# Kernel optimization log

Hardware: AMD Instinct MI355X
Metric: run time of the kernel (lower is better)

## Reference

```python
import jax, jax.numpy as jnp
import numpy as np

B, M, D = 8, 1024, 1024
H = 16
HD = D // H  # 64
F = 4096

def layer_norm(x, gamma, beta, eps=1e-5):
    mu = jnp.mean(x, axis=-1, keepdims=True)
    var = jnp.var(x, axis=-1, keepdims=True)
    return (x - mu) * jax.lax.rsqrt(var + eps) * gamma + beta

def setup_inputs() -> dict:
    key = jax.random.key(0)
    ks = jax.random.split(key, 16)
    s = 0.02
    return {
        "h": jax.random.normal(ks[0], (B, M, D), jnp.float32),
        "h_all": jax.random.normal(ks[1], (B, M, D), jnp.float32),
        "Wq": jax.random.normal(ks[2], (D, D), jnp.float32) * s,
        "Wk": jax.random.normal(ks[3], (D, D), jnp.float32) * s,
        "Wv": jax.random.normal(ks[4], (D, D), jnp.float32) * s,
        "Wo": jax.random.normal(ks[5], (D, D), jnp.float32) * s,
        "W1": jax.random.normal(ks[6], (D, F), jnp.float32) * s,
        "b1": jnp.zeros((F,), jnp.float32),
        "W2": jax.random.normal(ks[7], (F, D), jnp.float32) * s,
        "b2": jnp.zeros((D,), jnp.float32),
        "g1": jnp.ones((D,), jnp.float32),
        "be1": jnp.zeros((D,), jnp.float32),
        "g2": jnp.ones((D,), jnp.float32),
        "be2": jnp.zeros((D,), jnp.float32),
    }

def reference(h, h_all, Wq, Wk, Wv, Wo, W1, b1, W2, b2, g1, be1, g2, be2):
    Bx, Mx, Dx = h.shape
    # projections (no bias, per nn.Linear(bias=False))
    q = (h @ Wq).reshape(Bx, Mx, H, HD)        # [B,M,H,hd]
    k = (h_all @ Wk).reshape(Bx, -1, H, HD)    # [B,N,H,hd]
    v = (h_all @ Wv).reshape(Bx, -1, H, HD)
    # attention: scale by sqrt(head_dim) as in SeqAttention(hidden_size=head_dim)
    scores = jnp.einsum('bqhd,bkhd->bhqk', q, k) / jnp.sqrt(jnp.float32(HD))
    attn = jax.nn.softmax(scores, axis=-1)
    ctx = jnp.einsum('bhqk,bkhd->bqhd', attn, v).reshape(Bx, Mx, Dx)
    attn_out = ctx @ Wo
    # post-norm residual 1
    h1 = layer_norm(h + attn_out, g1, be1)
    # FFN
    ff = jax.nn.relu(h1 @ W1 + b1) @ W2 + b2
    # post-norm residual 2
    out = layer_norm(h1 + ff, g2, be2)
    return out
```

## Files before the change

### kernel.cpp

```cpp
#include <hip/hip_runtime.h>
#include <hip/hip_bf16.h>

#define ROWS 8192
#define DD   1024
#define HH   16
#define HD   64
#define FF   4096

typedef __attribute__((ext_vector_type(4))) float f32x4;
typedef __attribute__((ext_vector_type(8))) __bf16 bf16x8;
typedef __attribute__((ext_vector_type(8))) short short8v;

static __device__ __forceinline__ unsigned short f2bf(float f) {
  unsigned u = __float_as_uint(f);
  u += 0x7fffu + ((u >> 16) & 1u);
  return (unsigned short)(u >> 16);
}

static __device__ __forceinline__ f32x4 mfma16(bf16x8 a, bf16x8 b, f32x4 c) {
  return __builtin_amdgcn_mfma_f32_16x16x32_bf16(a, b, c, 0, 0, 0);
}

#define GLOAD16(gp, lp) __builtin_amdgcn_global_load_lds( \
    (__attribute__((address_space(1))) void*)(gp), \
    (__attribute__((address_space(3))) void*)(lp), 16, 0, 0)

__global__ __launch_bounds__(256) void cast_bf16_k(
    const float* __restrict__ in, unsigned short* __restrict__ out, int n4) {
  int i = blockIdx.x * 256 + threadIdx.x;
  if (i >= n4) return;
  float4 v = ((const float4*)in)[i];
  ushort4 o;
  o.x = f2bf(v.x); o.y = f2bf(v.y); o.z = f2bf(v.z); o.w = f2bf(v.w);
  ((ushort4*)out)[i] = o;
}

__global__ __launch_bounds__(256) void transpose_cast_k(
    const float* __restrict__ in, unsigned short* __restrict__ out, int R, int C) {
  __shared__ float tile[32][33];
  int bx = blockIdx.x * 32;
  int by = blockIdx.y * 32;
  int tx = threadIdx.x, ty = threadIdx.y;
  #pragma unroll
  for (int i = 0; i < 32; i += 8)
    tile[ty + i][tx] = in[(size_t)(by + ty + i) * C + bx + tx];
  __syncthreads();
  #pragma unroll
  for (int i = 0; i < 32; i += 8)
    out[(size_t)(bx + ty + i) * R + by + tx] = f2bf(tile[tx][ty + i]);
}

template <int BM, int MODE>
__global__ __launch_bounds__(512, 2) void gemm256(
    const unsigned short* __restrict__ A, const unsigned short* __restrict__ BT,
    const float* __restrict__ bias, void* __restrict__ Cout,
    int Ni, int Ki, int nbx) {
  constexpr int LA = BM / 64;
  constexpr int MR = BM / 32;
  constexpr int VN = LA + 4;
  __shared__ unsigned short As[2][BM * 64];
  __shared__ unsigned short Bs[2][256 * 64];

  const int tid  = threadIdx.x;
  const int lane = tid & 63;
  const int wid  = tid >> 6;
  const int wm   = wid >> 2;
  const int wn   = wid & 3;
  const int lr   = lane & 15;
  const int kq   = lane >> 4;
  const int axor = (lr & 7) << 4;

  const int nwg = gridDim.x;
  const int cpx = nwg >> 3;
  const int wg  = (int)blockIdx.x;
  const int swz = (wg & 7) * cpx + (wg >> 3);
  const int bx = swz % nbx, by = swz / nbx;
  const int brow = by * BM, bcol = bx * 256;

  const int srow = wid * 8 + (lane >> 3);
  const int scol = ((lane & 7) * 8) ^ ((srow & 7) << 3);
  size_t offA[LA], offB[4];
  #pragma unroll
  for (int L = 0; L < LA; ++L)
    offA[L] = (size_t)(brow + L * 64 + srow) * Ki + scol;
  #pragma unroll
  for (int L = 0; L < 4; ++L)
    offB[L] = (size_t)(bcol + L * 64 + srow) * Ki + scol;

  auto stage = [&](int t, int d) {
    #pragma unroll
    for (int L = 0; L < LA; ++L)
      GLOAD16(A + offA[L] + t * 64, (char*)As[d] + L * 8192 + wid * 1024);
    #pragma unroll
    for (int L = 0; L < 4; ++L)
      GLOAD16(BT + offB[L] + t * 64, (char*)Bs[d] + L * 8192 + wid * 1024);
  };

  f32x4 acc[MR][4] = {};
  const int NT = Ki >> 6;

  stage(0, 0);
  stage(1, 1);

  #pragma unroll 1
  for (int t = 0; t < NT; ++t) {
    const int d = t & 1;
    if constexpr (BM == 256) asm volatile("s_waitcnt vmcnt(8)" ::: "memory");
    else                     asm volatile("s_waitcnt vmcnt(6)" ::: "memory");
    __builtin_amdgcn_s_barrier();
    __builtin_amdgcn_sched_barrier(0);

    const unsigned short* as = As[d];
    const unsigned short* bs = Bs[d];
    #pragma unroll
    for (int kk = 0; kk < 2; ++kk) {
      bf16x8 af[MR], bfv[4];
      #pragma unroll
      for (int m = 0; m < MR; ++m)
        af[m] = *(const bf16x8*)((const char*)as +
            (wm * (BM / 2) + m * 16 + lr) * 128 + ((kk * 64 + kq * 16) ^ axor));
      #pragma unroll
      for (int n = 0; n < 4; ++n)
        bfv[n] = *(const bf16x8*)((const char*)bs +
            (wn * 64 + n * 16 + lr) * 128 + ((kk * 64 + kq * 16) ^ axor));
      #pragma unroll
      for (int m = 0; m < MR; ++m)
        #pragma unroll
        for (int n = 0; n < 4; ++n)
          acc[m][n] = mfma16(af[m], bfv[n], acc[m][n]);
    }

    __builtin_amdgcn_s_barrier();
    __builtin_amdgcn_sched_barrier(0);
    const int ts = (t + 2 < NT) ? t + 2 : NT - 1;
    stage(ts, d);
  }

  #pragma unroll
  for (int m = 0; m < MR; ++m) {
    #pragma unroll
    for (int n = 0; n < 4; ++n) {
      const int r0 = brow + wm * (BM / 2) + m * 16 + kq * 4;
      const int c  = bcol + wn * 64 + n * 16 + lr;
      const float bv = (MODE == 2 || MODE == 3) ? bias[c] : 0.0f;
      #pragma unroll
      for (int e = 0; e < 4; ++e) {
        float v = acc[m][n][e] + bv;
        if (MODE == 2) v = fmaxf(v, 0.0f);
        if (MODE == 0 || MODE == 2)
          ((unsigned short*)Cout)[(size_t)(r0 + e) * Ni + c] = f2bf(v);
        else
          ((float*)Cout)[(size_t)(r0 + e) * Ni + c] = v;
      }
    }
  }
}

__global__ __launch_bounds__(256, 2) void attn_k(
    const unsigned short* __restrict__ q, const unsigned short* __restrict__ kv,
    unsigned short* __restrict__ ctx) {
  __shared__ unsigned short Ks[64 * 64];
  __shared__ unsigned short Vt[64 * 64];
  __shared__ unsigned short Ps[4][16 * 64];
  const int tid = threadIdx.x;
  const int lane = tid & 63;
  const int wid = tid >> 6;
  const int bh = blockIdx.y;
  const int b = bh >> 4, h = bh & 15;
  const int qrow0 = blockIdx.x * 64 + wid * 16;
  const size_t tokbase = (size_t)b * 1024;

  bf16x8 aq[2];
  {
    const unsigned short* qp =
        q + (size_t)(tokbase + qrow0 + (lane & 15)) * DD + h * 64 + (lane >> 4) * 8;
    aq[0] = *(const bf16x8*)qp;
    aq[1] = *(const bf16x8*)(qp + 32);
  }

  float l_part[4] = {0.f, 0.f, 0.f, 0.f};
  f32x4 acc[4] = {};
  const float C = 0.125f * 1.4426950408889634f;

  for (int kt = 0; kt < 16; ++kt) {
    __syncthreads();
    #pragma unroll
    for (int it = 0; it < 2; ++it) {
      int r = (it * 4 + wid) * 8 + (lane >> 3);
      int cb = ((lane & 7) * 8) ^ ((r & 7) << 3);
      GLOAD16(kv + (size_t)(tokbase + kt * 64 + r) * 2048 + h * 64 + cb,
              (char*)Ks + (it * 4 + wid) * 1024);
    }
    #pragma unroll
    for (int it = 0; it < 2; ++it) {
      int tok = it * 32 + (tid >> 3);
      int d0 = (tid & 7) * 8;
      short8v vv = *(const short8v*)(kv + (size_t)(tokbase + kt * 64 + tok) * 2048 +
                                     1024 + h * 64 + d0);
      #pragma unroll
      for (int e = 0; e < 8; ++e) {
        int d = d0 + e;
        int sw = ((d & 7) ^ ((d >> 3) & 7)) & 7;
        *(unsigned short*)((char*)Vt + (((d * 128 + tok * 2) ^ (sw << 4)))) =
            (unsigned short)vv[e];
      }
    }
    __syncthreads();

    f32x4 sv[4] = {};
    #pragma unroll
    for (int jb = 0; jb < 4; ++jb)
      #pragma unroll
      for (int ks = 0; ks < 2; ++ks) {
        int row = jb * 16 + (lane & 15);
        bf16x8 bk = *(const bf16x8*)((const char*)Ks +
            ((row * 128 + ks * 64 + (lane >> 4) * 16) ^ ((row & 7) << 4)));
        sv[jb] = mfma16(aq[ks], bk, sv[jb]);
      }

    #pragma unroll
    for (int jb = 0; jb < 4; ++jb)
      #pragma unroll
      for (int j = 0; j < 4; ++j) {
        float p = exp2f(sv[jb][j] * C);
        sv[jb][j] = p;
        l_part[j] += p;
      }

    #pragma unroll
    for (int jb = 0; jb < 4; ++jb)
      #pragma unroll
      for (int j = 0; j < 4; ++j) {
        int row = (lane >> 4) * 4 + j;
        *(unsigned short*)((char*)Ps[wid] +
            ((row * 128 + (jb * 16 + (lane & 15)) * 2) ^ ((row & 7) << 4))) =
            f2bf(sv[jb][j]);
      }

    #pragma unroll
    for (int ks = 0; ks < 2; ++ks) {
      int prow = lane & 15;
      bf16x8 ap = *(const bf16x8*)((const char*)Ps[wid] +
          ((prow * 128 + ks * 64 + (lane >> 4) * 16) ^ ((prow & 7) << 4)));
      #pragma unroll
      for (int db = 0; db < 4; ++db) {
        int d = db * 16 + (lane & 15);
        int sw = ((d & 7) ^ ((d >> 3) & 7)) & 7;
        bf16x8 bv = *(const bf16x8*)((const char*)Vt +
            ((d * 128 + ks * 64 + (lane >> 4) * 16) ^ (sw << 4)));
        acc[db] = mfma16(ap, bv, acc[db]);
      }
    }
  }

  #pragma unroll
  for (int j = 0; j < 4; ++j) {
    float l = l_part[j];
    #pragma unroll
    for (int mk = 1; mk < 16; mk <<= 1) l += __shfl_xor(l, mk);
    float inv = 1.0f / l;
    int r = qrow0 + (lane >> 4) * 4 + j;
    #pragma unroll
    for (int db = 0; db < 4; ++db)
      ctx[(size_t)(tokbase + r) * DD + h * 64 + db * 16 + (lane & 15)] =
          f2bf(acc[db][j] * inv);
  }
}

template <int WB>
__global__ __launch_bounds__(256) void ln_add_k(
    const float* __restrict__ a, const float* __restrict__ b,
    const float* __restrict__ gamma, const float* __restrict__ beta,
    float* __restrict__ outf, unsigned short* __restrict__ outb) {
  int row = blockIdx.x;
  int tid = threadIdx.x;
  size_t base = (size_t)row * 1024 + tid * 4;
  float4 va = *(const float4*)(a + base);
  float4 vb = *(const float4*)(b + base);
  float x[4] = {va.x + vb.x, va.y + vb.y, va.z + vb.z, va.w + vb.w};
  float s = x[0] + x[1] + x[2] + x[3];
  float sq = x[0] * x[0] + x[1] * x[1] + x[2] * x[2] + x[3] * x[3];
  #pragma unroll
  for (int mk = 1; mk < 64; mk <<= 1) {
    s += __shfl_xor(s, mk);
    sq += __shfl_xor(sq, mk);
  }
  __shared__ float red[8];
  int wid = tid >> 6, lane = tid & 63;
  if (lane == 0) { red[wid] = s; red[4 + wid] = sq; }
  __syncthreads();
  s = red[0] + red[1] + red[2] + red[3];
  sq = red[4] + red[5] + red[6] + red[7];
  float mu = s * (1.0f / 1024.0f);
  float var = sq * (1.0f / 1024.0f) - mu * mu;
  float rs = rsqrtf(var + 1e-5f);
  float4 g = *(const float4*)(gamma + tid * 4);
  float4 be = *(const float4*)(beta + tid * 4);
  float y[4];
  y[0] = (x[0] - mu) * rs * g.x + be.x;
  y[1] = (x[1] - mu) * rs * g.y + be.y;
  y[2] = (x[2] - mu) * rs * g.z + be.z;
  y[3] = (x[3] - mu) * rs * g.w + be.w;
  float4 o; o.x = y[0]; o.y = y[1]; o.z = y[2]; o.w = y[3];
  *(float4*)(outf + base) = o;
  if (WB) {
    ushort4 ob;
    ob.x = f2bf(y[0]); ob.y = f2bf(y[1]); ob.z = f2bf(y[2]); ob.w = f2bf(y[3]);
    *(ushort4*)(outb + base) = ob;
  }
}

extern "C" void kernel_launch(void* const* d_in, const int* in_sizes, int n_in,
                              void* d_out, int out_size, void* d_ws, size_t ws_size,
                              hipStream_t stream) {
  const float* h    = (const float*)d_in[0];
  const float* hall = (const float*)d_in[1];
  const float* Wq   = (const float*)d_in[2];
  const float* Wk   = (const float*)d_in[3];
  const float* Wv   = (const float*)d_in[4];
  const float* Wo   = (const float*)d_in[5];
  const float* W1   = (const float*)d_in[6];
  const float* b1   = (const float*)d_in[7];
  const float* W2   = (const float*)d_in[8];
  const float* b2   = (const float*)d_in[9];
  const float* g1   = (const float*)d_in[10];
  const float* be1  = (const float*)d_in[11];
  const float* g2   = (const float*)d_in[12];
  const float* be2  = (const float*)d_in[13];

  char* ws = (char*)d_ws;
  size_t off = 0;
  auto alloc = [&](size_t n) { size_t o = off; off += (n + 255) & ~(size_t)255; return o; };
  const size_t hb_o   = alloc((size_t)ROWS * DD * 2);
  const size_t hab_o  = alloc((size_t)ROWS * DD * 2);
  const size_t wqt_o  = alloc((size_t)DD * DD * 2);
  const size_t wkvt_o = alloc((size_t)DD * DD * 4);
  const size_t wot_o  = alloc((size_t)DD * DD * 2);
  const size_t w1t_o  = alloc((size_t)DD * FF * 2);
  const size_t w2t_o  = alloc((size_t)FF * DD * 2);
  const size_t qb_o   = alloc((size_t)ROWS * DD * 2);
  const size_t kvb_o  = alloc((size_t)ROWS * DD * 4);
  const size_t cx_o   = alloc((size_t)ROWS * DD * 2);
  const size_t h1_o   = alloc((size_t)ROWS * DD * 4);
  const size_t h1b_o  = alloc((size_t)ROWS * DD * 2);

  unsigned short* hb   = (unsigned short*)(ws + hb_o);
  unsigned short* hab  = (unsigned short*)(ws + hab_o);
  unsigned short* wqt  = (unsigned short*)(ws + wqt_o);
  unsigned short* wkvt = (unsigned short*)(ws + wkvt_o);
  unsigned short* wot  = (unsigned short*)(ws + wot_o);
  unsigned short* w1t  = (unsigned short*)(ws + w1t_o);
  unsigned short* w2t  = (unsigned short*)(ws + w2t_o);
  unsigned short* qb   = (unsigned short*)(ws + qb_o);
  unsigned short* kvb  = (unsigned short*)(ws + kvb_o);
  unsigned short* cxb  = (unsigned short*)(ws + cx_o);
  float*          h1   = (float*)(ws + h1_o);
  unsigned short* h1b  = (unsigned short*)(ws + h1b_o);
  float*          attn_out = (float*)(ws + hb_o);
  unsigned short* ff1      = (unsigned short*)(ws + qb_o);
  float*          outf     = (float*)d_out;

  cast_bf16_k<<<ROWS * DD / 1024, 256, 0, stream>>>(h, hb, ROWS * DD / 4);
  cast_bf16_k<<<ROWS * DD / 1024, 256, 0, stream>>>(hall, hab, ROWS * DD / 4);
  dim3 tb(32, 8);
  transpose_cast_k<<<dim3(32, 32), tb, 0, stream>>>(Wq, wqt, DD, DD);
  transpose_cast_k<<<dim3(32, 32), tb, 0, stream>>>(Wk, wkvt, DD, DD);
  transpose_cast_k<<<dim3(32, 32), tb, 0, stream>>>(Wv, wkvt + (size_t)DD * DD, DD, DD);
  transpose_cast_k<<<dim3(32, 32), tb, 0, stream>>>(Wo, wot, DD, DD);
  transpose_cast_k<<<dim3(128, 32), tb, 0, stream>>>(W1, w1t, DD, FF);
  transpose_cast_k<<<dim3(32, 128), tb, 0, stream>>>(W2, w2t, FF, DD);

  gemm256<128, 0><<<dim3(64 * 4), 512, 0, stream>>>(hb,  wqt,  nullptr, qb,  DD,   DD, 4);
  gemm256<256, 0><<<dim3(32 * 8), 512, 0, stream>>>(hab, wkvt, nullptr, kvb, 2048, DD, 8);

  attn_k<<<dim3(16, 128), 256, 0, stream>>>(qb, kvb, cxb);

  gemm256<128, 1><<<dim3(64 * 4), 512, 0, stream>>>(cxb, wot, nullptr, attn_out, DD, DD, 4);
  ln_add_k<1><<<ROWS, 256, 0, stream>>>(h, attn_out, g1, be1, h1, h1b);

  gemm256<256, 2><<<dim3(32 * 16), 512, 0, stream>>>(h1b, w1t, b1, ff1, FF, DD, 16);
  gemm256<128, 3><<<dim3(64 * 4),  512, 0, stream>>>(ff1, w2t, b2, outf, DD, FF, 4);

  ln_add_k<0><<<ROWS, 256, 0, stream>>>(h1, outf, g2, be2, outf, nullptr);
}
```

Measured before the change: 411.9 us.

## Write V transposed from the KV GEMM and double-buffer K/V loads in attention

The KV projection GEMM gets a new epilogue mode that writes K row-major and V transposed per (batch, head) into separate buffers. This lets the attention kernel stage both K and V with async global-to-LDS loads instead of scalar LDS transposes. The attention kernel now uses 512-thread blocks covering 128 query rows, double-buffers K/V tiles with prefetch two steps ahead, and synchronises with explicit waitcnt and barriers. An lgkmcnt wait is also added before the GEMM barrier. The transposed V stores are 8-byte scattered writes, and the larger LDS footprint may limit occupancy.

```diff
diff --git a/kernel.cpp b/kernel.cpp
--- a/kernel.cpp
+++ b/kernel.cpp
@@ -9,7 +9,6 @@
 
 typedef __attribute__((ext_vector_type(4))) float f32x4;
 typedef __attribute__((ext_vector_type(8))) __bf16 bf16x8;
-typedef __attribute__((ext_vector_type(8))) short short8v;
 
 static __device__ __forceinline__ unsigned short f2bf(float f) {
   unsigned u = __float_as_uint(f);
@@ -53,11 +52,10 @@
 template <int BM, int MODE>
 __global__ __launch_bounds__(512, 2) void gemm256(
     const unsigned short* __restrict__ A, const unsigned short* __restrict__ BT,
-    const float* __restrict__ bias, void* __restrict__ Cout,
+    const float* __restrict__ bias, void* __restrict__ Cout, void* __restrict__ Cout2,
     int Ni, int Ki, int nbx) {
   constexpr int LA = BM / 64;
   constexpr int MR = BM / 32;
-  constexpr int VN = LA + 4;
   __shared__ unsigned short As[2][BM * 64];
   __shared__ unsigned short Bs[2][256 * 64];
 
@@ -130,6 +128,7 @@
           acc[m][n] = mfma16(af[m], bfv[n], acc[m][n]);
     }
 
+    asm volatile("s_waitcnt lgkmcnt(0)" ::: "memory");
     __builtin_amdgcn_s_barrier();
     __builtin_amdgcn_sched_barrier(0);
     const int ts = (t + 2 < NT) ? t + 2 : NT - 1;
@@ -142,38 +141,65 @@
     for (int n = 0; n < 4; ++n) {
       const int r0 = brow + wm * (BM / 2) + m * 16 + kq * 4;
       const int c  = bcol + wn * 64 + n * 16 + lr;
-      const float bv = (MODE == 2 || MODE == 3) ? bias[c] : 0.0f;
-      #pragma unroll
-      for (int e = 0; e < 4; ++e) {
-        float v = acc[m][n][e] + bv;
-        if (MODE == 2) v = fmaxf(v, 0.0f);
-        if (MODE == 0 || MODE == 2)
-          ((unsigned short*)Cout)[(size_t)(r0 + e) * Ni + c] = f2bf(v);
-        else
-          ((float*)Cout)[(size_t)(r0 + e) * Ni + c] = v;
+      if constexpr (MODE == 4) {
+        if (c < 1024) {
+          #pragma unroll
+          for (int e = 0; e < 4; ++e)
+            ((unsigned short*)Cout)[(size_t)(r0 + e) * 1024 + c] = f2bf(acc[m][n][e]);
+        } else {
+          const int cc = c - 1024;
+          const int bq = r0 >> 10;
+          const int tok = r0 & 1023;
+          ushort4 pk;
+          pk.x = f2bf(acc[m][n][0]); pk.y = f2bf(acc[m][n][1]);
+          pk.z = f2bf(acc[m][n][2]); pk.w = f2bf(acc[m][n][3]);
+          *(ushort4*)((unsigned short*)Cout2 + ((size_t)bq * 1024 + cc) * 1024 + tok) = pk;
+        }
+      } else {
+        const float bv = (MODE == 2 || MODE == 3) ? bias[c] : 0.0f;
+        #pragma unroll
+        for (int e = 0; e < 4; ++e) {
+          float v = acc[m][n][e] + bv;
+          if (MODE == 2) v = fmaxf(v, 0.0f);
+          if (MODE == 0 || MODE == 2)
+            ((unsigned short*)Cout)[(size_t)(r0 + e) * Ni + c] = f2bf(v);
+          else
+            ((float*)Cout)[(size_t)(r0 + e) * Ni + c] = v;
+        }
       }
     }
   }
 }
 
-__global__ __launch_bounds__(256, 2) void attn_k(
-    const unsigned short* __restrict__ q, const unsigned short* __restrict__ kv,
-    unsigned short* __restrict__ ctx) {
-  __shared__ unsigned short Ks[64 * 64];
-  __shared__ unsigned short Vt[64 * 64];
-  __shared__ unsigned short Ps[4][16 * 64];
+__global__ __launch_bounds__(512, 4) void attn_k(
+    const unsigned short* __restrict__ q, const unsigned short* __restrict__ k,
+    const unsigned short* __restrict__ vT, unsigned short* __restrict__ ctx) {
+  __shared__ unsigned short Ks[2][64 * 64];
+  __shared__ unsigned short Vt[2][64 * 64];
+  __shared__ unsigned short Ps[8][16 * 64];
   const int tid = threadIdx.x;
   const int lane = tid & 63;
   const int wid = tid >> 6;
   const int bh = blockIdx.y;
   const int b = bh >> 4, h = bh & 15;
-  const int qrow0 = blockIdx.x * 64 + wid * 16;
+  const int qrow0 = blockIdx.x * 128 + wid * 16;
   const size_t tokbase = (size_t)b * 1024;
+  const int lr = lane & 15, kq = lane >> 4;
+
+  const int srow = tid >> 3;
+  const int scol = ((tid & 7) * 8) ^ ((srow & 7) << 3);
+  const unsigned short* kg = k + (tokbase + srow) * 1024 + h * 64 + scol;
+  const unsigned short* vg = vT + ((size_t)(b * 16 + h) * 64 + srow) * 1024 + scol;
+  const int ldst = tid * 16;
+
+  auto stage = [&](int kt, int d) {
+    GLOAD16(kg + (size_t)kt * 64 * 1024, (char*)Ks[d] + ldst);
+    GLOAD16(vg + kt * 64, (char*)Vt[d] + ldst);
+  };
 
   bf16x8 aq[2];
   {
-    const unsigned short* qp =
-        q + (size_t)(tokbase + qrow0 + (lane & 15)) * DD + h * 64 + (lane >> 4) * 8;
+    const unsigned short* qp = q + (tokbase + qrow0 + lr) * DD + h * 64 + kq * 8;
     aq[0] = *(const bf16x8*)qp;
     aq[1] = *(const bf16x8*)(qp + 32);
   }
@@ -182,39 +208,24 @@
   f32x4 acc[4] = {};
   const float C = 0.125f * 1.4426950408889634f;
 
+  stage(0, 0);
+  stage(1, 1);
+
+  #pragma unroll 2
   for (int kt = 0; kt < 16; ++kt) {
-    __syncthreads();
-    #pragma unroll
-    for (int it = 0; it < 2; ++it) {
-      int r = (it * 4 + wid) * 8 + (lane >> 3);
-      int cb = ((lane & 7) * 8) ^ ((r & 7) << 3);
-      GLOAD16(kv + (size_t)(tokbase + kt * 64 + r) * 2048 + h * 64 + cb,
-              (char*)Ks + (it * 4 + wid) * 1024);
-    }
-    #pragma unroll
-    for (int it = 0; it < 2; ++it) {
-      int tok = it * 32 + (tid >> 3);
-      int d0 = (tid & 7) * 8;
-      short8v vv = *(const short8v*)(kv + (size_t)(tokbase + kt * 64 + tok) * 2048 +
-                                     1024 + h * 64 + d0);
-      #pragma unroll
-      for (int e = 0; e < 8; ++e) {
-        int d = d0 + e;
-        int sw = ((d & 7) ^ ((d >> 3) & 7)) & 7;
-        *(unsigned short*)((char*)Vt + (((d * 128 + tok * 2) ^ (sw << 4)))) =
-            (unsigned short)vv[e];
-      }
-    }
-    __syncthreads();
+    const int d = kt & 1;
+    asm volatile("s_waitcnt vmcnt(2)" ::: "memory");
+    __builtin_amdgcn_s_barrier();
+    __builtin_amdgcn_sched_barrier(0);
 
     f32x4 sv[4] = {};
     #pragma unroll
     for (int jb = 0; jb < 4; ++jb)
       #pragma unroll
       for (int ks = 0; ks < 2; ++ks) {
-        int row = jb * 16 + (lane & 15);
-        bf16x8 bk = *(const bf16x8*)((const char*)Ks +
-            ((row * 128 + ks * 64 + (lane >> 4) * 16) ^ ((row & 7) << 4)));
+        int row = jb * 16 + lr;
+        bf16x8 bk = *(const bf16x8*)((const char*)Ks[d] +
+            row * 128 + ((ks * 64 + kq * 16) ^ ((row & 7) << 4)));
         sv[jb] = mfma16(aq[ks], bk, sv[jb]);
       }
 
@@ -231,26 +242,29 @@
     for (int jb = 0; jb < 4; ++jb)
       #pragma unroll
       for (int j = 0; j < 4; ++j) {
-        int row = (lane >> 4) * 4 + j;
+        int row = kq * 4 + j;
         *(unsigned short*)((char*)Ps[wid] +
-            ((row * 128 + (jb * 16 + (lane & 15)) * 2) ^ ((row & 7) << 4))) =
-            f2bf(sv[jb][j]);
+            ((row * 128 + (jb * 16 + lr) * 2) ^ ((row & 7) << 4))) = f2bf(sv[jb][j]);
       }
 
     #pragma unroll
     for (int ks = 0; ks < 2; ++ks) {
-      int prow = lane & 15;
       bf16x8 ap = *(const bf16x8*)((const char*)Ps[wid] +
-          ((prow * 128 + ks * 64 + (lane >> 4) * 16) ^ ((prow & 7) << 4)));
+          lr * 128 + ((ks * 64 + kq * 16) ^ ((lr & 7) << 4)));
       #pragma unroll
       for (int db = 0; db < 4; ++db) {
-        int d = db * 16 + (lane & 15);
-        int sw = ((d & 7) ^ ((d >> 3) & 7)) & 7;
-        bf16x8 bv = *(const bf16x8*)((const char*)Vt +
-            ((d * 128 + ks * 64 + (lane >> 4) * 16) ^ (sw << 4)));
+        int dd = db * 16 + lr;
+        bf16x8 bv = *(const bf16x8*)((const char*)Vt[d] +
+            dd * 128 + ((ks * 64 + kq * 16) ^ ((dd & 7) << 4)));
         acc[db] = mfma16(ap, bv, acc[db]);
       }
     }
+
+    asm volatile("s_waitcnt lgkmcnt(0)" ::: "memory");
+    __builtin_amdgcn_s_barrier();
+    __builtin_amdgcn_sched_barrier(0);
+    const int ts = (kt + 2 < 16) ? kt + 2 : 15;
+    stage(ts, d);
   }
 
   #pragma unroll
@@ -259,11 +273,10 @@
     #pragma unroll
     for (int mk = 1; mk < 16; mk <<= 1) l += __shfl_xor(l, mk);
     float inv = 1.0f / l;
-    int r = qrow0 + (lane >> 4) * 4 + j;
+    int r = qrow0 + kq * 4 + j;
     #pragma unroll
     for (int db = 0; db < 4; ++db)
-      ctx[(size_t)(tokbase + r) * DD + h * 64 + db * 16 + (lane & 15)] =
-          f2bf(acc[db][j] * inv);
+      ctx[(tokbase + r) * DD + h * 64 + db * 16 + lr] = f2bf(acc[db][j] * inv);
   }
 }
 
@@ -339,7 +352,8 @@
   const size_t w1t_o  = alloc((size_t)DD * FF * 2);
   const size_t w2t_o  = alloc((size_t)FF * DD * 2);
   const size_t qb_o   = alloc((size_t)ROWS * DD * 2);
-  const size_t kvb_o  = alloc((size_t)ROWS * DD * 4);
+  const size_t kb_o   = alloc((size_t)ROWS * DD * 2);
+  const size_t vt_o   = alloc((size_t)ROWS * DD * 2);
   const size_t cx_o   = alloc((size_t)ROWS * DD * 2);
   const size_t h1_o   = alloc((size_t)ROWS * DD * 4);
   const size_t h1b_o  = alloc((size_t)ROWS * DD * 2);
@@ -352,7 +366,8 @@
   unsigned short* w1t  = (unsigned short*)(ws + w1t_o);
   unsigned short* w2t  = (unsigned short*)(ws + w2t_o);
   unsigned short* qb   = (unsigned short*)(ws + qb_o);
-  unsigned short* kvb  = (unsigned short*)(ws + kvb_o);
+  unsigned short* kb   = (unsigned short*)(ws + kb_o);
+  unsigned short* vTb  = (unsigned short*)(ws + vt_o);
   unsigned short* cxb  = (unsigned short*)(ws + cx_o);
   float*          h1   = (float*)(ws + h1_o);
   unsigned short* h1b  = (unsigned short*)(ws + h1b_o);
@@ -370,16 +385,16 @@
   transpose_cast_k<<<dim3(128, 32), tb, 0, stream>>>(W1, w1t, DD, FF);
   transpose_cast_k<<<dim3(32, 128), tb, 0, stream>>>(W2, w2t, FF, DD);
 
-  gemm256<128, 0><<<dim3(64 * 4), 512, 0, stream>>>(hb,  wqt,  nullptr, qb,  DD,   DD, 4);
-  gemm256<256, 0><<<dim3(32 * 8), 512, 0, stream>>>(hab, wkvt, nullptr, kvb, 2048, DD, 8);
-
-  attn_k<<<dim3(16, 128), 256, 0, stream>>>(qb, kvb, cxb);
-
-  gemm256<128, 1><<<dim3(64 * 4), 512, 0, stream>>>(cxb, wot, nullptr, attn_out, DD, DD, 4);
+  gemm256<128, 0><<<dim3(256), 512, 0, stream>>>(hb,  wqt,  nullptr, qb, nullptr, DD,   DD, 4);
+  gemm256<256, 4><<<dim3(256), 512, 0, stream>>>(hab, wkvt, nullptr, kb, vTb,    2048, DD, 8);
+
+  attn_k<<<dim3(8, 128), 512, 0, stream>>>(qb, kb, vTb, cxb);
+
+  gemm256<128, 1><<<dim3(256), 512, 0, stream>>>(cxb, wot, nullptr, attn_out, nullptr, DD, DD, 4);
   ln_add_k<1><<<ROWS, 256, 0, stream>>>(h, attn_out, g1, be1, h1, h1b);
 
-  gemm256<256, 2><<<dim3(32 * 16), 512, 0, stream>>>(h1b, w1t, b1, ff1, FF, DD, 16);
-  gemm256<128, 3><<<dim3(64 * 4),  512, 0, stream>>>(ff1, w2t, b2, outf, DD, FF, 4);
+  gemm256<256, 2><<<dim3(512), 512, 0, stream>>>(h1b, w1t, b1, ff1, nullptr, FF, DD, 16);
+  gemm256<128, 3><<<dim3(256), 512, 0, stream>>>(ff1, w2t, b2, outf, nullptr, DD, FF, 4);
 
   ln_add_k<0><<<ROWS, 256, 0, stream>>>(h1, outf, g2, be2, outf, nullptr);
 }
```

New measurement: 398.8 us. 1.03x faster.
